# Performance work log

Measured on AMD Instinct MI355X. Metric: run time of the kernel, lower is better.

Reference implementation:

```python
import jax, jax.numpy as jnp
import numpy as np
from jax import lax

N = 2048
NUM_CLASSES = 21  # background + 20 classes


def xy_to_cxcy(xy):
    return jnp.concatenate([(xy[:, 2:] + xy[:, :2]) / 2.0, xy[:, 2:] - xy[:, :2]], axis=-1)


def cxcy_to_xy(c):
    return jnp.concatenate([c[:, :2] - c[:, 2:] / 2.0, c[:, :2] + c[:, 2:] / 2.0], axis=-1)


def gcxgcy_to_cxcy(g, priors_cxcy):
    # offsets already pre-scaled (/10, /20) by the caller, matching the torch forward
    return jnp.concatenate([g[:, :2] * priors_cxcy[:, 2:] + priors_cxcy[:, :2],
                            jnp.exp(g[:, 2:]) * priors_cxcy[:, 2:]], axis=-1)


def pairwise_iou(a, b):
    # a: [N,4], b: [M,4] corner format -> [N,M]
    lt = jnp.maximum(a[:, None, :2], b[None, :, :2])
    rb = jnp.minimum(a[:, None, 2:], b[None, :, 2:])
    wh = jnp.clip(rb - lt, 0.0)
    inter = wh[..., 0] * wh[..., 1]
    area_a = (a[:, 2] - a[:, 0]) * (a[:, 3] - a[:, 1])
    area_b = (b[:, 2] - b[:, 0]) * (b[:, 3] - b[:, 1])
    return inter / (area_a[:, None] + area_b[None, :] - inter)


def _detect(rois_xy, predicted_locs, predicted_scores, min_score, max_overlap, top_k):
    n = rois_xy.shape[0]
    rois_cxcy = xy_to_cxcy(rois_xy)
    locs = predicted_locs.reshape(n, -1, 4)                      # [N, C, 4]
    probs = jax.nn.softmax(predicted_scores, axis=1)             # [N, C]
    best = jnp.argmax(probs, axis=1)                             # locs for argmax class
    g = jnp.take_along_axis(locs, best[:, None, None], axis=1)[:, 0, :]
    g = jnp.concatenate([g[:, :2] / 10.0, g[:, 2:] / 20.0], axis=-1)
    decoded = cxcy_to_xy(gcxgcy_to_cxcy(g, rois_cxcy))           # [N, 4]

    def nms_class(cls_scores):
        valid = cls_scores > min_score
        s = jnp.where(valid, cls_scores, -jnp.inf)
        order = jnp.argsort(-s)                                  # desc; invalid last
        s_sorted = s[order]
        b_sorted = decoded[order]
        ov = lax.stop_gradient(pairwise_iou(b_sorted, b_sorted))  # [N, N]
        sup0 = ~valid[order]                                     # invalid start suppressed

        def body(i, sup):
            new = jnp.logical_or(sup, ov[i] > max_overlap)
            new = new.at[i].set(False)                           # never self-suppress
            return jnp.where(sup[i], sup, new)                   # skip already-suppressed

        sup = lax.fori_loop(0, n, body, sup0)
        return b_sorted, jnp.where(~sup, s_sorted, -jnp.inf)

    # vmap the greedy NMS over the 20 foreground classes
    boxes_c, scores_c = jax.vmap(nms_class)(probs[:, 1:].T)      # [20,N,4], [20,N]
    labels_c = jnp.broadcast_to(jnp.arange(1, NUM_CLASSES)[:, None], scores_c.shape)

    fs = scores_c.reshape(-1)
    fb = boxes_c.reshape(-1, 4)
    fl = labels_c.reshape(-1)
    topv, topi = lax.top_k(fs, top_k)
    ok = jnp.isfinite(topv)
    out_boxes = jnp.where(ok[:, None], fb[topi],
                          jnp.array([0.0, 0.0, 1.0, 1.0], dtype=fb.dtype))
    out_labels = jnp.where(ok, fl[topi], 0)
    out_scores = jnp.where(ok, topv, 0.0)
    return out_boxes, out_labels, out_scores


def setup_inputs() -> dict:
    key = jax.random.key(0)
    k1, k2, k3, k4 = jax.random.split(key, 4)
    cxcy = jax.random.uniform(k1, (N, 2), minval=0.1, maxval=0.9)
    wh = jax.random.uniform(k2, (N, 2), minval=0.05, maxval=0.3)
    rois_xy = jnp.concatenate([cxcy - wh / 2.0, cxcy + wh / 2.0], axis=-1)
    predicted_locs = jax.random.normal(k3, (N, NUM_CLASSES * 4), dtype=jnp.float32) * 0.5
    predicted_scores = jax.random.normal(k4, (N, NUM_CLASSES), dtype=jnp.float32) * 2.0
    return {"rois_xy": rois_xy,
            "predicted_locs": predicted_locs,
            "predicted_scores": predicted_scores,
            "min_score": jnp.float32(0.01),
            "max_overlap": jnp.float32(0.45),
            "top_k": 100}


def reference(rois_xy, predicted_locs, predicted_scores, min_score, max_overlap, top_k):
    return _detect(rois_xy, predicted_locs, predicted_scores, min_score, max_overlap, top_k)
```

## Files before the change

kernel.cpp:

```cpp
#include <hip/hip_runtime.h>
#include <cstdint>

#define NROI 2048
#define NCLS 21
#define NFG  20
#define CPAD 128
#define CTOT (NFG * CPAD)
#define NTHR 1024
#define SBLK 256
#define RSEL 480
#define SCAP 512
#define CSEL 512
#define INVH 0xFF800000u

typedef unsigned long long u64;
typedef unsigned int u32;

__device__ __forceinline__ u32 desc_key(float s) {
  u32 u = __float_as_uint(s);
  u32 asc = (u & 0x80000000u) ? ~u : (u | 0x80000000u);
  return ~asc;
}
__device__ __forceinline__ float key_to_float(u32 desc) {
  u32 asc = ~desc;
  u32 u = (asc & 0x80000000u) ? (asc ^ 0x80000000u) : ~asc;
  return __uint_as_float(u);
}
__device__ __forceinline__ u64 shflx_u64(u64 v, int m) {
  u32 lo = (u32)v, hi = (u32)(v >> 32);
  lo = (u32)__shfl_xor((int)lo, m);
  hi = (u32)__shfl_xor((int)hi, m);
  return ((u64)hi << 32) | (u64)lo;
}
__device__ __forceinline__ void cmpex64(u64& mine, u64 other, int i, int j, int k) {
  bool amIlow = ((i & j) == 0);
  bool dir = ((i & k) == 0);
  bool otherLess = other < mine;
  if (otherLess != (amIlow != dir)) mine = other;
}

__device__ __forceinline__ void bucket_select(const int* h, int need, int lane,
                                              int* outB, int* outC) {
  int base = lane << 2;
  int c0 = h[base], c1 = h[base + 1], c2 = h[base + 2], c3 = h[base + 3];
  int s = c0 + c1 + c2 + c3;
  int pre = s;
  #pragma unroll
  for (int off = 1; off < 64; off <<= 1) {
    int v = __shfl_up(pre, off);
    if (lane >= off) pre += v;
  }
  u64 ball = __ballot(pre >= need);
  int ln = __ffsll((long long)ball) - 1;
  int exc = __shfl(pre, ln) - __shfl(s, ln);
  int b0 = __shfl(c0, ln), b1 = __shfl(c1, ln), b2 = __shfl(c2, ln);
  int bkt, cb;
  if (exc + b0 >= need)                { bkt = (ln << 2) + 0; cb = exc; }
  else if (exc + b0 + b1 >= need)      { bkt = (ln << 2) + 1; cb = exc + b0; }
  else if (exc + b0 + b1 + b2 >= need) { bkt = (ln << 2) + 2; cb = exc + b0 + b1; }
  else                                 { bkt = (ln << 2) + 3; cb = exc + b0 + b1 + b2; }
  if (lane == 0) { *outB = bkt; *outC = cb; }
}

__global__ __launch_bounds__(NTHR)
void k_nms(const float* __restrict__ rois,
           const float* __restrict__ locs,
           const float* __restrict__ scores,
           const float* __restrict__ min_score_p,
           const float* __restrict__ max_overlap_p,
           u64* __restrict__ cand,
           float4* __restrict__ cbox,
           u32* __restrict__ done,
           float* __restrict__ out,
           const int* __restrict__ top_k_p) {
  __shared__ u32 LDSW[12800];
  __shared__ u64 remInitW[4];
  __shared__ int hist1[256], hist2[256];
  __shared__ int cntLds, scLds, cSelSh, selB1, selC1, selB2, selD2, mSh, cCnt;
  __shared__ u32 lastSh;

  u64* mbAu    = (u64*)(LDSW + 0);
  u64* mbBu    = (u64*)(LDSW + 1024);
  u64* skeyW64 = (u64*)(LDSW + 2048);
  u64* maskW   = (u64*)(LDSW + 3072);
  float* bx0   = (float*)(LDSW + 5120);
  float* by0   = (float*)(LDSW + 5376);
  float* bx1   = (float*)(LDSW + 5632);
  float* by1   = (float*)(LDSW + 5888);
  float* areaA = (float*)(LDSW + 6144);
  float* sx0   = (float*)(LDSW + 6400);
  float* sy0   = (float*)(LDSW + 6528);
  float* sx1   = (float*)(LDSW + 6656);
  float* sy1   = (float*)(LDSW + 6784);
  float* sarea = (float*)(LDSW + 6912);
  u32* survKeyH = LDSW + 7040;
  u32* survRows = LDSW + 7168;
  float* wx0 = (float*)(LDSW + 7296);
  float* wy0 = (float*)(LDSW + 7808);
  float* wx1 = (float*)(LDSW + 8320);
  float* wy1 = (float*)(LDSW + 8832);
  float* stgF  = (float*)LDSW;
  u32* keyCol  = LDSW + 10752;

  const int cls = blockIdx.x;
  const int cc = cls + 1;
  const int tid = threadIdx.x;
  const int lane = tid & 63;
  const int wid = tid >> 6;
  const float msc = *min_score_p;
  const float ovr = *max_overlap_p;
  const int K = *top_k_p;
  const int Kcap = (K < CPAD) ? K : CPAD;

  if (tid == 0) { cntLds = 0; scLds = 0; }

  for (int chunk = 0; chunk < 4; ++chunk) {
    const float* src = scores + (size_t)chunk * 512 * NCLS;
    for (int t = tid; t < 512 * NCLS; t += NTHR) stgF[t] = src[t];
    __syncthreads();
    if (tid < 512) {
      const float* row = stgF + tid * NCLS;
      float s[NCLS];
      #pragma unroll
      for (int c = 0; c < NCLS; ++c) s[c] = row[c];
      float m = s[0];
      #pragma unroll
      for (int c = 0; c < NCLS; ++c) m = fmaxf(m, s[c]);
      float sum = 0.0f;
      #pragma unroll
      for (int c = 0; c < NCLS; ++c) { s[c] = expf(s[c] - m); sum += s[c]; }
      float ec = s[0];
      #pragma unroll
      for (int c = 1; c < NCLS; ++c) ec = (c == cc) ? s[c] : ec;
      float p = ec / sum;
      keyCol[chunk * 512 + tid] = desc_key((p > msc) ? p : -__builtin_inff());
    }
    __syncthreads();
  }

  u32 h0k = keyCol[tid], h1k = keyCol[tid + 1024];
  u64 kq0 = ((u64)h0k << 32) | (u32)tid;
  u64 kq1 = ((u64)h1k << 32) | (u32)(tid + 1024);
  {
    u64 ba = __ballot(h0k < INVH), bb = __ballot(h1k < INVH);
    if (lane == 0) atomicAdd(&cntLds, __popcll(ba) + __popcll(bb));
  }
  __syncthreads();
  const int nv = cntLds;

  int sc = 0;
  int processed = 0;
  u64 minKey = 0ULL;

  while (sc < Kcap && processed < nv) {
    int rem = nv - processed;
    int need = (rem < RSEL) ? rem : RSEL;

    if (tid < 256) { hist1[tid] = 0; hist2[tid] = 0; }
    if (tid == 0) cSelSh = 0;
    __syncthreads();
    bool val0 = (kq0 > minKey) && ((u32)(kq0 >> 32) < INVH);
    bool val1 = (kq1 > minKey) && ((u32)(kq1 >> 32) < INVH);
    if (val0) atomicAdd(&hist1[(int)((kq0 >> 56) & 255)], 1);
    if (val1) atomicAdd(&hist1[(int)((kq1 >> 56) & 255)], 1);
    __syncthreads();
    if (wid == 0) bucket_select(hist1, need, lane, &selB1, &selC1);
    __syncthreads();
    const int B1 = selB1, C1 = selC1;
    if (val0 && (int)((kq0 >> 56) & 255) == B1)
      atomicAdd(&hist2[(int)((kq0 >> 48) & 255)], 1);
    if (val1 && (int)((kq1 >> 56) & 255) == B1)
      atomicAdd(&hist2[(int)((kq1 >> 48) & 255)], 1);
    __syncthreads();
    if (wid == 0) bucket_select(hist2, need - C1, lane, &selB2, &selD2);
    __syncthreads();
    const int pred16 = (selB1 << 8) | selB2;

    bool s0 = val0 && (int)((kq0 >> 48) & 0xFFFF) <= pred16;
    bool s1 = val1 && (int)((kq1 >> 48) & 0xFFFF) <= pred16;
    {
      u64 b0 = __ballot(s0), b1 = __ballot(s1);
      int cnt = __popcll(b0) + __popcll(b1);
      int basePos = 0;
      if (lane == 0) basePos = cnt ? atomicAdd(&cSelSh, cnt) : 0;
      basePos = __shfl(basePos, 0);
      u64 lm = (1ULL << lane) - 1ULL;
      int p0 = basePos + __popcll(b0 & lm);
      int p1 = basePos + __popcll(b0) + __popcll(b1 & lm);
      if (s0 && p0 < SCAP) mbAu[p0] = kq0;
      if (s1 && p1 < SCAP) mbAu[p1] = kq1;
    }
    __syncthreads();
    int Csel = cSelSh; if (Csel > SCAP) Csel = SCAP;
    if (tid < SCAP && tid >= Csel) mbAu[tid] = ~0ULL;
    __syncthreads();

    u64 key = (tid < SCAP) ? mbAu[tid] : ~0ULL;
    int parity = 0;
    auto ldsp = [&](int k, int j) {
      u64* buf = parity ? mbBu : mbAu; parity ^= 1;
      if (tid < SCAP) buf[tid] = key;
      __syncthreads();
      if (tid < SCAP) { u64 o = buf[tid ^ j]; cmpex64(key, o, tid, j, k); }
    };
    auto shfp = [&](int k, int j) {
      if (tid < SCAP) { u64 o = shflx_u64(key, j); cmpex64(key, o, tid, j, k); }
    };
    for (int k = 2; k <= 64; k <<= 1)
      for (int j = k >> 1; j >= 1; j >>= 1) shfp(k, j);
    ldsp(128, 64);
    for (int j = 32; j >= 1; j >>= 1) shfp(128, j);
    ldsp(256, 128); ldsp(256, 64);
    for (int j = 32; j >= 1; j >>= 1) shfp(256, j);
    ldsp(512, 256); ldsp(512, 128); ldsp(512, 64);
    for (int j = 32; j >= 1; j >>= 1) shfp(512, j);
    if (tid < SCAP) skeyW64[tid] = key;

    if (tid < SCAP && tid < Csel) {
      int row = (int)(u32)key;
      const float* sr = scores + row * NCLS;
      float s[NCLS];
      #pragma unroll
      for (int c = 0; c < NCLS; ++c) s[c] = sr[c];
      float m = s[0];
      #pragma unroll
      for (int c = 0; c < NCLS; ++c) m = fmaxf(m, s[c]);
      float sum = 0.0f;
      #pragma unroll
      for (int c = 0; c < NCLS; ++c) { s[c] = expf(s[c] - m); sum += s[c]; }
      float pb = s[0] / sum; int best = 0;
      #pragma unroll
      for (int c = 1; c < NCLS; ++c) {
        float p = s[c] / sum;
        if (p > pb) { pb = p; best = c; }
      }
      float4 roi = ((const float4*)rois)[row];
      float pcx = __fmul_rn(__fadd_rn(roi.x, roi.z), 0.5f);
      float pcy = __fmul_rn(__fadd_rn(roi.y, roi.w), 0.5f);
      float pw  = __fsub_rn(roi.z, roi.x);
      float ph  = __fsub_rn(roi.w, roi.y);
      float4 gl = ((const float4*)locs)[row * NCLS + best];
      float g0 = gl.x / 10.0f;
      float g1 = gl.y / 10.0f;
      float g2 = gl.z / 20.0f;
      float g3 = gl.w / 20.0f;
      float cx = __fadd_rn(__fmul_rn(g0, pw), pcx);
      float cy = __fadd_rn(__fmul_rn(g1, ph), pcy);
      float w  = __fmul_rn(expf(g2), pw);
      float h  = __fmul_rn(expf(g3), ph);
      float hw = __fmul_rn(w, 0.5f);
      float hh = __fmul_rn(h, 0.5f);
      wx0[tid] = __fsub_rn(cx, hw);
      wy0[tid] = __fsub_rn(cy, hh);
      wx1[tid] = __fadd_rn(cx, hw);
      wy1[tid] = __fadd_rn(cy, hh);
    }
    __syncthreads();

    for (int base = 0; base < Csel && sc < Kcap; base += SBLK) {
      int RL = Csel - base; if (RL > SBLK) RL = SBLK;
      if (tid < SBLK) {
        int p = base + tid; if (p > Csel - 1) p = Csel - 1;
        float x0v = wx0[p], y0v = wy0[p], x1v = wx1[p], y1v = wy1[p];
        bx0[tid] = x0v; by0[tid] = y0v; bx1[tid] = x1v; by1[tid] = y1v;
        areaA[tid] = __fmul_rn(__fsub_rn(x1v, x0v), __fsub_rn(y1v, y0v));
      }
      if (tid < 4) remInitW[tid] = 0ULL;
      __syncthreads();

      if (sc > 0 && tid < SBLK) {
        float jx0 = bx0[tid], jy0 = by0[tid], jx1 = bx1[tid], jy1 = by1[tid];
        float ab = areaA[tid];
        bool kill = false;
        for (int u = 0; u < sc; ++u) {
          float ix0 = sx0[u], iy0 = sy0[u], ix1 = sx1[u], iy1 = sy1[u];
          float ia = sarea[u];
          float lx = fmaxf(ix0, jx0), ly = fmaxf(iy0, jy0);
          float rx = fminf(ix1, jx1), ry = fminf(iy1, jy1);
          float w_ = fmaxf(__fsub_rn(rx, lx), 0.0f);
          float h_ = fmaxf(__fsub_rn(ry, ly), 0.0f);
          float inter = __fmul_rn(w_, h_);
          float iou = __fdiv_rn(inter, __fsub_rn(__fadd_rn(ia, ab), inter));
          kill = kill || (iou > ovr);
        }
        u64 bal = __ballot(kill);
        if (lane == 0) remInitW[wid] = bal;
      }
      __syncthreads();

      {
        int nw = (RL + 63) >> 6;
        for (int r2 = wid; r2 < RL; r2 += 16) {
          if ((remInitW[r2 >> 6] >> (r2 & 63)) & 1ULL) continue;
          float ix0 = bx0[r2], iy0 = by0[r2], ix1 = bx1[r2], iy1 = by1[r2];
          float ia = areaA[r2];
          for (int ct = (r2 >> 6); ct < nw; ++ct) {
            int j = (ct << 6) + lane;
            float jx0 = bx0[j], jy0 = by0[j], jx1 = bx1[j], jy1 = by1[j];
            float ab = areaA[j];
            float lx = fmaxf(ix0, jx0), ly = fmaxf(iy0, jy0);
            float rx = fminf(ix1, jx1), ry = fminf(iy1, jy1);
            float w_ = fmaxf(__fsub_rn(rx, lx), 0.0f);
            float h_ = fmaxf(__fsub_rn(ry, ly), 0.0f);
            float inter = __fmul_rn(w_, h_);
            float iou = __fdiv_rn(inter, __fsub_rn(__fadd_rn(ia, ab), inter));
            bool bit = iou > ovr;
            if (ct == (r2 >> 6)) bit = bit && (j > r2);
            u64 bal = __ballot(bit);
            if (lane == 0) maskW[(r2 << 2) + ct] = bal;
          }
        }
      }
      __syncthreads();

      if (wid == 0) {
        int t0 = RL;
        u64 rw0 = (t0 <= 0) ? ~0ULL : ((t0 >= 64) ? 0ULL : (~0ULL << t0));
        int t1 = t0 - 64;
        u64 rw1 = (t1 <= 0) ? ~0ULL : ((t1 >= 64) ? 0ULL : (~0ULL << t1));
        int t2 = t0 - 128;
        u64 rw2 = (t2 <= 0) ? ~0ULL : ((t2 >= 64) ? 0ULL : (~0ULL << t2));
        int t3 = t0 - 192;
        u64 rw3 = (t3 <= 0) ? ~0ULL : ((t3 >= 64) ? 0ULL : (~0ULL << t3));
        rw0 |= remInitW[0]; rw1 |= remInitW[1];
        rw2 |= remInitW[2]; rw3 |= remInitW[3];
        int scW = sc;
        bool full = scW >= Kcap;
        u64 a00,a01,a02,a03,a10,a11,a12,a13,a20,a21,a22,a23,a30,a31,a32,a33;
        u64 b00,b01,b02,b03,b10,b11,b12,b13,b20,b21,b22,b23,b30,b31,b32,b33;
#define LD4(V0,V1,V2,V3,R) { int rr_ = (R); \
        V0 = maskW[(rr_<<2)+0]; V1 = maskW[(rr_<<2)+1]; \
        V2 = maskW[(rr_<<2)+2]; V3 = maskW[(rr_<<2)+3]; }
#define PRX(RWG, BIT, M0,M1,M2,M3, ROW) \
        if (!full && !(((RWG) >> (BIT)) & 1ULL)) { \
          rw0 |= (M0); rw1 |= (M1); rw2 |= (M2); rw3 |= (M3); \
          if (lane == 0) survRows[scW] = (u32)(base + (ROW)); \
          ++scW; full = (scW >= Kcap); \
        }
#define SWEEPG(G, RWG) \
        if (!full && (((G) << 6) < RL)) { \
          const int rb = (G) << 6; \
          LD4(a00,a01,a02,a03, rb+0) LD4(a10,a11,a12,a13, rb+1) \
          LD4(a20,a21,a22,a23, rb+2) LD4(a30,a31,a32,a33, rb+3) \
          for (int bb = 0; bb < 64 && !full; bb += 4) { \
            LD4(b00,b01,b02,b03, rb+bb+4) LD4(b10,b11,b12,b13, rb+bb+5) \
            LD4(b20,b21,b22,b23, rb+bb+6) LD4(b30,b31,b32,b33, rb+bb+7) \
            PRX(RWG, bb+0, a00,a01,a02,a03, rb+bb+0) \
            PRX(RWG, bb+1, a10,a11,a12,a13, rb+bb+1) \
            PRX(RWG, bb+2, a20,a21,a22,a23, rb+bb+2) \
            PRX(RWG, bb+3, a30,a31,a32,a33, rb+bb+3) \
            a00=b00;a01=b01;a02=b02;a03=b03; a10=b10;a11=b11;a12=b12;a13=b13; \
            a20=b20;a21=b21;a22=b22;a23=b23; a30=b30;a31=b31;a32=b32;a33=b33; \
          } \
        }
        SWEEPG(0, rw0) SWEEPG(1, rw1) SWEEPG(2, rw2) SWEEPG(3, rw3)
#undef SWEEPG
#undef PRX
#undef LD4
        if (lane == 0) scLds = scW;
      }
      __syncthreads();

      {
        int scNew = scLds;
        if (tid >= sc && tid < scNew) {
          int wrow = (int)survRows[tid];
          int rr = wrow - base;
          sx0[tid] = bx0[rr]; sy0[tid] = by0[rr];
          sx1[tid] = bx1[rr]; sy1[tid] = by1[rr];
          sarea[tid] = areaA[rr];
          survKeyH[tid] = (u32)(skeyW64[wrow] >> 32);
        }
        __syncthreads();
        sc = scNew;
      }
    }

    minKey = skeyW64[Csel - 1];
    processed += Csel;
    __syncthreads();
  }

  if (tid < CPAD) {
    int o = cls * CPAD + tid;
    if (tid < sc) {
      cand[o] = ((u64)survKeyH[tid] << 32) | (u32)o;
      cbox[o] = make_float4(sx0[tid], sy0[tid], sx1[tid], sy1[tid]);
    } else {
      cand[o] = ~0ULL;
    }
  }

  __threadfence();
  __syncthreads();
  if (tid == 0) lastSh = atomicAdd(done, 1u);
  __syncthreads();
  if (lastSh != NFG - 1) return;
  __threadfence();

  u64* kk = (u64*)LDSW;
  u64* ck = (u64*)(LDSW + 5120);
  if (tid == 0) cCnt = 0;
  if (tid < 256) { hist1[tid] = 0; hist2[tid] = 0; }
  __syncthreads();
  for (int t = tid; t < CTOT; t += NTHR) {
    u64 v = cand[t];
    kk[t] = v;
    if (v != ~0ULL) atomicAdd(&hist1[(int)(v >> 56)], 1);
  }
  __syncthreads();
  if (wid == 0) {
    int b4 = lane << 2;
    int s = hist1[b4] + hist1[b4 + 1] + hist1[b4 + 2] + hist1[b4 + 3];
    #pragma unroll
    for (int off = 32; off; off >>= 1) s += __shfl_xor(s, off);
    if (lane == 0) mSh = s;
  }
  __syncthreads();
  const int M = mSh;
  const int Kneed = (K < M) ? K : M;

  if (Kneed > 0) {
    if (wid == 0) bucket_select(hist1, Kneed, lane, &selB1, &selC1);
    __syncthreads();
    const int B1 = selB1, C1 = selC1;
    for (int t = tid; t < CTOT; t += NTHR) {
      u64 v = kk[t];
      if (v != ~0ULL && (int)(v >> 56) == B1)
        atomicAdd(&hist2[(int)((v >> 48) & 255)], 1);
    }
    __syncthreads();
    if (wid == 0) bucket_select(hist2, Kneed - C1, lane, &selB2, &selD2);
    __syncthreads();
    const int B2 = selB2;
    for (int t = tid; t < CTOT; t += NTHR) {
      u64 v = kk[t];
      if (v == ~0ULL) continue;
      int b1 = (int)(v >> 56);
      int b2 = (int)((v >> 48) & 255);
      if (b1 < B1 || (b1 == B1 && b2 <= B2)) {
        int pos = atomicAdd(&cCnt, 1);
        if (pos < CSEL) ck[pos] = v;
      }
    }
    __syncthreads();
    const int C = cCnt;
    if (C <= CSEL) {
      if (tid < C) {
        u64 my = ck[tid];
        int rank = 0;
        for (int u = 0; u < C; ++u) rank += (ck[u] < my) ? 1 : 0;
        if (rank < K) {
          u32 flat = (u32)(my & 0xFFFFFFFFu);
          float score = key_to_float((u32)(my >> 32));
          int c2 = (int)(flat >> 7);
          float4 b = cbox[flat];
          out[rank * 4 + 0] = b.x;
          out[rank * 4 + 1] = b.y;
          out[rank * 4 + 2] = b.z;
          out[rank * 4 + 3] = b.w;
          out[K * 4 + rank] = (float)(c2 + 1);
          out[K * 5 + rank] = score;
        }
      }
    } else {
      for (int t = tid; t < CTOT; t += NTHR) {
        u64 kap = kk[t];
        if (kap == ~0ULL) continue;
        int rank = 0;
        #pragma unroll
        for (int cc2 = 0; cc2 < NFG; ++cc2) {
          const u64* a = kk + cc2 * CPAD;
          int lb = 0;
          #pragma unroll
          for (int s2 = CPAD >> 1; s2; s2 >>= 1) {
            int pq = lb + s2;
            if (a[pq - 1] < kap) lb = pq;
          }
          rank += lb;
        }
        if (rank < K) {
          u32 flat = (u32)(kap & 0xFFFFFFFFu);
          float score = key_to_float((u32)(kap >> 32));
          int c2 = (int)(flat >> 7);
          float4 b = cbox[flat];
          out[rank * 4 + 0] = b.x;
          out[rank * 4 + 1] = b.y;
          out[rank * 4 + 2] = b.z;
          out[rank * 4 + 3] = b.w;
          out[K * 4 + rank] = (float)(c2 + 1);
          out[K * 5 + rank] = score;
        }
      }
    }
  }
  __syncthreads();
  for (int r = tid; r < K; r += NTHR) {
    if (r >= M) {
      out[r * 4 + 0] = 0.0f; out[r * 4 + 1] = 0.0f;
      out[r * 4 + 2] = 1.0f; out[r * 4 + 3] = 1.0f;
      out[K * 4 + r] = 0.0f;
      out[K * 5 + r] = 0.0f;
    }
  }
}

extern "C" void kernel_launch(void* const* d_in, const int* in_sizes, int n_in,
                              void* d_out, int out_size, void* d_ws, size_t ws_size,
                              hipStream_t stream) {
  const float* rois        = (const float*)d_in[0];
  const float* locs        = (const float*)d_in[1];
  const float* scores      = (const float*)d_in[2];
  const float* min_score   = (const float*)d_in[3];
  const float* max_overlap = (const float*)d_in[4];
  const int*   top_k       = (const int*)d_in[5];

  char* ws = (char*)d_ws;
  u64*    cand = (u64*)ws;
  float4* cbox = (float4*)(ws + 20480);
  u32*    done = (u32*)(ws + 20480 + 40960);

  hipMemsetAsync(done, 0, 4, stream);
  k_nms<<<NFG, NTHR, 0, stream>>>(rois, locs, scores, min_score, max_overlap,
                                  cand, cbox, done, (float*)d_out, top_k);
}
```

Measured before the change: 71.01 us.

## Split softmax across blocks and share class keys via global grid barrier

Each of the 20 blocks used to compute the softmax over all 2048 rows on its own and keep only its class's probability. Now each block computes the softmax for a 103-row slice and writes keys for every class into a transposed global buffer. A spin-wait barrier on a global counter holds every block until all slices are written, and then each block reads its class column. This removes 20-fold redundant softmax work and score loading, but adds a grid-wide barrier that relies on all 20 blocks being resident at once, plus extra global traffic.

```diff
diff --git a/kernel.cpp b/kernel.cpp
--- a/kernel.cpp
+++ b/kernel.cpp
@@ -11,6 +11,7 @@
 #define RSEL 480
 #define SCAP 512
 #define CSEL 512
+#define RPB  103
 #define INVH 0xFF800000u
 
 typedef unsigned long long u64;
@@ -70,10 +71,11 @@
            const float* __restrict__ max_overlap_p,
            u64* __restrict__ cand,
            float4* __restrict__ cbox,
-           u32* __restrict__ done,
+           u32* __restrict__ keyT,
+           u32* __restrict__ ctr,
            float* __restrict__ out,
            const int* __restrict__ top_k_p) {
-  __shared__ u32 LDSW[12800];
+  __shared__ u32 LDSW[9344];
   __shared__ u64 remInitW[4];
   __shared__ int hist1[256], hist2[256];
   __shared__ int cntLds, scLds, cSelSh, selB1, selC1, selB2, selD2, mSh, cCnt;
@@ -99,11 +101,9 @@
   float* wy0 = (float*)(LDSW + 7808);
   float* wx1 = (float*)(LDSW + 8320);
   float* wy1 = (float*)(LDSW + 8832);
-  float* stgF  = (float*)LDSW;
-  u32* keyCol  = LDSW + 10752;
+  float* stgF = (float*)LDSW;
 
   const int cls = blockIdx.x;
-  const int cc = cls + 1;
   const int tid = threadIdx.x;
   const int lane = tid & 63;
   const int wid = tid >> 6;
@@ -114,11 +114,13 @@
 
   if (tid == 0) { cntLds = 0; scLds = 0; }
 
-  for (int chunk = 0; chunk < 4; ++chunk) {
-    const float* src = scores + (size_t)chunk * 512 * NCLS;
-    for (int t = tid; t < 512 * NCLS; t += NTHR) stgF[t] = src[t];
-    __syncthreads();
-    if (tid < 512) {
+  {
+    const int rb0 = cls * RPB;
+    int rcount = NROI - rb0; if (rcount > RPB) rcount = RPB;
+    for (int t = tid; t < rcount * NCLS; t += NTHR)
+      stgF[t] = scores[(size_t)rb0 * NCLS + t];
+    __syncthreads();
+    if (tid < rcount) {
       const float* row = stgF + tid * NCLS;
       float s[NCLS];
       #pragma unroll
@@ -129,16 +131,30 @@
       float sum = 0.0f;
       #pragma unroll
       for (int c = 0; c < NCLS; ++c) { s[c] = expf(s[c] - m); sum += s[c]; }
-      float ec = s[0];
-      #pragma unroll
-      for (int c = 1; c < NCLS; ++c) ec = (c == cc) ? s[c] : ec;
-      float p = ec / sum;
-      keyCol[chunk * 512 + tid] = desc_key((p > msc) ? p : -__builtin_inff());
-    }
-    __syncthreads();
-  }
-
-  u32 h0k = keyCol[tid], h1k = keyCol[tid + 1024];
+      #pragma unroll
+      for (int c = 1; c < NCLS; ++c) {
+        float p = s[c] / sum;
+        keyT[(c - 1) * NROI + rb0 + tid] =
+            desc_key((p > msc) ? p : -__builtin_inff());
+      }
+    }
+    __threadfence();
+    __syncthreads();
+    if (tid == 0) {
+      atomicAdd(&ctr[1], 1u);
+      u32 v;
+      do {
+        __builtin_amdgcn_s_sleep(8);
+        v = __hip_atomic_load(&ctr[1], __ATOMIC_ACQUIRE,
+                              __HIP_MEMORY_SCOPE_AGENT);
+      } while (v < (u32)NFG);
+    }
+    __syncthreads();
+    __threadfence();
+  }
+
+  u32 h0k = keyT[cls * NROI + tid];
+  u32 h1k = keyT[cls * NROI + tid + 1024];
   u64 kq0 = ((u64)h0k << 32) | (u32)tid;
   u64 kq1 = ((u64)h1k << 32) | (u32)(tid + 1024);
   {
@@ -393,7 +409,7 @@
 
   __threadfence();
   __syncthreads();
-  if (tid == 0) lastSh = atomicAdd(done, 1u);
+  if (tid == 0) lastSh = atomicAdd(&ctr[0], 1u);
   __syncthreads();
   if (lastSh != NFG - 1) return;
   __threadfence();
@@ -518,9 +534,10 @@
   char* ws = (char*)d_ws;
   u64*    cand = (u64*)ws;
   float4* cbox = (float4*)(ws + 20480);
-  u32*    done = (u32*)(ws + 20480 + 40960);
-
-  hipMemsetAsync(done, 0, 4, stream);
+  u32*    keyT = (u32*)(ws + 20480 + 40960);
+  u32*    ctr  = (u32*)(ws + 20480 + 40960 + 163840);
+
+  hipMemsetAsync(ctr, 0, 8, stream);
   k_nms<<<NFG, NTHR, 0, stream>>>(rois, locs, scores, min_score, max_overlap,
-                                  cand, cbox, done, (float*)d_out, top_k);
-}
+                                  cand, cbox, keyT, ctr, (float*)d_out, top_k);
+}
```

New measurement: 73.90 us. +4.1%, slower.
